# Kernel tuning notes

Hardware: AMD Instinct MI355X
Metric: run time of the kernel (lower is better)

## Reference

```python
import jax, jax.numpy as jnp
import numpy as np

B, T, D = 32, 2048, 128


def setup_inputs() -> dict:
    key = jax.random.key(0)
    k1, k2, k3 = jax.random.split(key, 3)
    values = jax.random.normal(k1, (B, T, D), dtype=jnp.float32)
    # monotonically increasing per-feature timestamps (irregular sampling)
    times = jnp.cumsum(jax.random.uniform(k2, (B, T, D), dtype=jnp.float32), axis=1)
    mask = jax.random.randint(k3, (B, T, D), 0, 2) > 0  # True = observed
    return {"values": values, "times": times, "mask": mask}


def _fill(x, t, mask):
    """Parallel forward fill (LOCF) and backward fill (NOCB) of x and t.

    Replaces the serial Keras RNN scan with cummax/cummin over observation
    indices followed by a gather. Matches ForwardCell semantics:
      forward : x init 0, t init times[:, 0, :]
      backward: x init 0, t init max(times, axis=1)
    """
    Tn = x.shape[1]
    ar = jnp.broadcast_to(jnp.arange(Tn, dtype=jnp.int32)[None, :, None], x.shape)
    # ---- forward fill ----
    fidx = jax.lax.cummax(jnp.where(mask, ar, -1), axis=1)  # last observed idx
    fvalid = fidx >= 0
    fi = jnp.clip(fidx, 0, Tn - 1)
    x_last = jnp.where(fvalid, jnp.take_along_axis(x, fi, axis=1), 0.0)
    t_last = jnp.where(fvalid, jnp.take_along_axis(t, fi, axis=1), t[:, :1, :])
    # ---- backward fill ----
    bidx = jax.lax.cummin(jnp.where(mask, ar, Tn), axis=1, reverse=True)  # next observed idx
    bvalid = bidx < Tn
    bi = jnp.clip(bidx, 0, Tn - 1)
    x_next = jnp.where(bvalid, jnp.take_along_axis(x, bi, axis=1), 0.0)
    t_next = jnp.where(bvalid, jnp.take_along_axis(t, bi, axis=1),
                       jnp.max(t, axis=1, keepdims=True))
    return x_last, t_last, x_next, t_next


def reference(values, times, mask):
    x_last, t_last, x_next, t_next = _fill(values, times, mask)
    denom = t_next - t_last
    num = x_last * (t_next - times) + x_next * (times - t_last)
    safe = denom != 0.0
    x_itp = num / jnp.where(safe, denom, 1.0)
    x_itp = jnp.where(safe & jnp.isfinite(x_itp), x_itp, 0.0)  # nan/inf -> 0
    return jnp.where(mask, values, x_itp)
```

## Files before the change

### kernel.cpp

```cpp
#include <hip/hip_runtime.h>
#include <math.h>

constexpr int B = 32;
constexpr int T = 2048;
constexpr int D = 128;

__global__ __launch_bounds__(256)
void interp_wide_kernel(const float* __restrict__ values,
                        const float* __restrict__ times,
                        const int*   __restrict__ mask,
                        float*       __restrict__ out)
{
    const int gid = blockIdx.x * 256 + threadIdx.x;
    const int d4 = gid & 31;
    const int c  = (gid >> 5) & 511;
    const int b  = gid >> 14;
    const int d0 = d4 << 2;
    const int t0 = c << 2;

    const size_t bbase = (size_t)b * T * D;
    const float* vrow = values + bbase + (size_t)t0 * D + d0;
    const float* trow = times  + bbase + (size_t)t0 * D + d0;
    const int*   mrow = mask   + bbase + (size_t)t0 * D + d0;

    float vv[4][4], tt[4][4];
    unsigned mb[4] = {0u, 0u, 0u, 0u};
#pragma unroll
    for (int i = 0; i < 4; ++i) {
        const float4 a = *reinterpret_cast<const float4*>(vrow + i * D);
        const float4 s = *reinterpret_cast<const float4*>(trow + i * D);
        const int4   m = *reinterpret_cast<const int4*>(mrow + i * D);
        vv[i][0] = a.x; vv[i][1] = a.y; vv[i][2] = a.z; vv[i][3] = a.w;
        tt[i][0] = s.x; tt[i][1] = s.y; tt[i][2] = s.z; tt[i][3] = s.w;
        mb[0] |= (m.x != 0 ? 1u : 0u) << i;
        mb[1] |= (m.y != 0 ? 1u : 0u) << i;
        mb[2] |= (m.z != 0 ? 1u : 0u) << i;
        mb[3] |= (m.w != 0 ? 1u : 0u) << i;
    }

    unsigned fw[4] = {0u, 0u, 0u, 0u};
    unsigned bw[4] = {0u, 0u, 0u, 0u};
#pragma unroll
    for (int k = 0; k < 16; ++k) {
        const int st = t0 - 16 + k;
        if (st >= 0) {
            const int4 m = *reinterpret_cast<const int4*>(
                mask + bbase + (size_t)st * D + d0);
            fw[0] |= (m.x != 0 ? 1u : 0u) << k;
            fw[1] |= (m.y != 0 ? 1u : 0u) << k;
            fw[2] |= (m.z != 0 ? 1u : 0u) << k;
            fw[3] |= (m.w != 0 ? 1u : 0u) << k;
        }
    }
#pragma unroll
    for (int k = 0; k < 16; ++k) {
        const int st = t0 + 4 + k;
        if (st < T) {
            const int4 m = *reinterpret_cast<const int4*>(
                mask + bbase + (size_t)st * D + d0);
            bw[0] |= (m.x != 0 ? 1u : 0u) << k;
            bw[1] |= (m.y != 0 ? 1u : 0u) << k;
            bw[2] |= (m.z != 0 ? 1u : 0u) << k;
            bw[3] |= (m.w != 0 ? 1u : 0u) << k;
        }
    }

    int fi[4], bi[4];
#pragma unroll
    for (int j = 0; j < 4; ++j) {
        fi[j] = fw[j] ? (t0 - 16 + (31 - __builtin_clz(fw[j]))) : -1;
        bi[j] = bw[j] ? (t0 + 4 + __builtin_ctz(bw[j])) : -1;
    }
#pragma unroll
    for (int j = 0; j < 4; ++j) {
        if (fi[j] < 0 && t0 > 16) {
            for (int st = t0 - 17; st >= 0; --st) {
                if (mask[bbase + (size_t)st * D + d0 + j] != 0) { fi[j] = st; break; }
            }
        }
        if (bi[j] < 0 && t0 + 20 < T) {
            for (int st = t0 + 20; st < T; ++st) {
                if (mask[bbase + (size_t)st * D + d0 + j] != 0) { bi[j] = st; break; }
            }
        }
    }

    float fx[4], ft[4], bx[4], bt[4];
#pragma unroll
    for (int j = 0; j < 4; ++j) {
        const int sF = fi[j] < 0 ? 0 : fi[j];
        const int sB = bi[j] < 0 ? 0 : bi[j];
        const size_t oF = bbase + (size_t)sF * D + d0 + j;
        const size_t oB = bbase + (size_t)sB * D + d0 + j;
        fx[j] = values[oF]; ft[j] = times[oF];
        bx[j] = values[oB]; bt[j] = times[oB];
    }
    const float4 tf4 = *reinterpret_cast<const float4*>(times + bbase + d0);
    const float4 tl4 = *reinterpret_cast<const float4*>(
        times + bbase + (size_t)(T - 1) * D + d0);
    const float tfirst[4] = {tf4.x, tf4.y, tf4.z, tf4.w};
    const float tlastT[4] = {tl4.x, tl4.y, tl4.z, tl4.w};
#pragma unroll
    for (int j = 0; j < 4; ++j) {
        if (fi[j] < 0) { fx[j] = 0.f; ft[j] = tfirst[j]; }
        if (bi[j] < 0) { bx[j] = 0.f; bt[j] = tlastT[j]; }
    }

    float res[4][4];
#pragma unroll
    for (int j = 0; j < 4; ++j) {
        float xl[4], tl[4];
        float cfx = fx[j], cft = ft[j];
#pragma unroll
        for (int i = 0; i < 4; ++i) {
            if ((mb[j] >> i) & 1u) { cfx = vv[i][j]; cft = tt[i][j]; }
            xl[i] = cfx; tl[i] = cft;
        }
        float cbx = bx[j], cbt = bt[j];
#pragma unroll
        for (int i = 3; i >= 0; --i) {
            const bool obs = (mb[j] >> i) & 1u;
            if (obs) { cbx = vv[i][j]; cbt = tt[i][j]; }
            const float denom = cbt - tl[i];
            const float num   = xl[i] * (cbt - tt[i][j]) + cbx * (tt[i][j] - tl[i]);
            const bool  safe  = (denom != 0.f);
            float xi = num / (safe ? denom : 1.f);
            xi = (safe && isfinite(xi)) ? xi : 0.f;
            res[i][j] = obs ? vv[i][j] : xi;
        }
    }

    float* orow = out + bbase + (size_t)t0 * D + d0;
#pragma unroll
    for (int i = 0; i < 4; ++i) {
        float4 o; o.x = res[i][0]; o.y = res[i][1]; o.z = res[i][2]; o.w = res[i][3];
        *reinterpret_cast<float4*>(orow + i * D) = o;
    }
}

extern "C" void kernel_launch(void* const* d_in, const int* in_sizes, int n_in,
                              void* d_out, int out_size, void* d_ws, size_t ws_size,
                              hipStream_t stream)
{
    const float* values = (const float*)d_in[0];
    const float* times  = (const float*)d_in[1];
    const int*   mask   = (const int*)d_in[2];
    float*       out    = (float*)d_out;

    const int total_threads = B * (T / 4) * (D / 4);
    interp_wide_kernel<<<total_threads / 256, 256, 0, stream>>>(values, times, mask, out);
}
```

Before: 161.3 us.

## Share halo mask window through LDS bitmasks instead of per-thread global rescans

Each block now covers 32 timesteps by 128 features and loads the mask window, including a 16-step halo on each side, from global memory once. It packs the window into per-feature 64-bit bitmasks in shared memory, and each thread finds its previous and next observation with clz/ctz. Before, every thread reloaded 32 mask rows on its own. The change also drops the separate first/last time loads by gathering directly from index 0 or T-1. In exchange it adds two block barriers and shared-memory traffic.

```diff
diff --git a/kernel.cpp b/kernel.cpp
--- a/kernel.cpp
+++ b/kernel.cpp
@@ -1,109 +1,120 @@
 #include <hip/hip_runtime.h>
 #include <math.h>
 
-constexpr int B = 32;
-constexpr int T = 2048;
-constexpr int D = 128;
+constexpr int B    = 32;
+constexpr int T    = 2048;
+constexpr int D    = 128;
+constexpr int TG   = 32;
+constexpr int HALO = 16;
+constexpr int WIN  = 64;
+constexpr int APAD = 17;
 
 __global__ __launch_bounds__(256)
-void interp_wide_kernel(const float* __restrict__ values,
-                        const float* __restrict__ times,
-                        const int*   __restrict__ mask,
-                        float*       __restrict__ out)
+void interp_lds_kernel(const float* __restrict__ values,
+                       const float* __restrict__ times,
+                       const int*   __restrict__ mask,
+                       float*       __restrict__ out)
 {
-    const int gid = blockIdx.x * 256 + threadIdx.x;
-    const int d4 = gid & 31;
-    const int c  = (gid >> 5) & 511;
-    const int b  = gid >> 14;
-    const int d0 = d4 << 2;
-    const int t0 = c << 2;
+    __shared__ unsigned char A[D * APAD];
+    __shared__ unsigned      W[2][D];
+
+    const int tid   = threadIdx.x;
+    const int blk   = blockIdx.x;
+    const int b     = blk >> 6;
+    const int tg    = blk & 63;
+    const int t_blk = tg * TG;
+    const int w0    = t_blk - HALO;
 
     const size_t bbase = (size_t)b * T * D;
+
+    const int d4    = tid & 31;
+    const int c_loc = tid >> 5;
+    const int d0    = d4 << 2;
+    const int t0    = t_blk + (c_loc << 2);
+
+    float vv[4][4], tt[4][4];
     const float* vrow = values + bbase + (size_t)t0 * D + d0;
     const float* trow = times  + bbase + (size_t)t0 * D + d0;
-    const int*   mrow = mask   + bbase + (size_t)t0 * D + d0;
-
-    float vv[4][4], tt[4][4];
-    unsigned mb[4] = {0u, 0u, 0u, 0u};
 #pragma unroll
     for (int i = 0; i < 4; ++i) {
         const float4 a = *reinterpret_cast<const float4*>(vrow + i * D);
         const float4 s = *reinterpret_cast<const float4*>(trow + i * D);
-        const int4   m = *reinterpret_cast<const int4*>(mrow + i * D);
         vv[i][0] = a.x; vv[i][1] = a.y; vv[i][2] = a.z; vv[i][3] = a.w;
         tt[i][0] = s.x; tt[i][1] = s.y; tt[i][2] = s.z; tt[i][3] = s.w;
-        mb[0] |= (m.x != 0 ? 1u : 0u) << i;
-        mb[1] |= (m.y != 0 ? 1u : 0u) << i;
-        mb[2] |= (m.z != 0 ? 1u : 0u) << i;
-        mb[3] |= (m.w != 0 ? 1u : 0u) << i;
     }
 
-    unsigned fw[4] = {0u, 0u, 0u, 0u};
-    unsigned bw[4] = {0u, 0u, 0u, 0u};
 #pragma unroll
-    for (int k = 0; k < 16; ++k) {
-        const int st = t0 - 16 + k;
-        if (st >= 0) {
-            const int4 m = *reinterpret_cast<const int4*>(
-                mask + bbase + (size_t)st * D + d0);
-            fw[0] |= (m.x != 0 ? 1u : 0u) << k;
-            fw[1] |= (m.y != 0 ? 1u : 0u) << k;
-            fw[2] |= (m.z != 0 ? 1u : 0u) << k;
-            fw[3] |= (m.w != 0 ? 1u : 0u) << k;
+    for (int k = 0; k < 2; ++k) {
+        const int task = tid + k * 256;
+        const int td4  = task & 31;
+        const int ts4  = task >> 5;
+        const int tdd  = td4 << 2;
+        unsigned n0 = 0, n1 = 0, n2 = 0, n3 = 0;
+#pragma unroll
+        for (int i = 0; i < 4; ++i) {
+            const int st = w0 + (ts4 << 2) + i;
+            if (st >= 0 && st < T) {
+                const int4 m = *reinterpret_cast<const int4*>(
+                    mask + bbase + (size_t)st * D + tdd);
+                n0 |= (m.x != 0 ? 1u : 0u) << i;
+                n1 |= (m.y != 0 ? 1u : 0u) << i;
+                n2 |= (m.z != 0 ? 1u : 0u) << i;
+                n3 |= (m.w != 0 ? 1u : 0u) << i;
+            }
         }
+        A[(tdd + 0) * APAD + ts4] = (unsigned char)n0;
+        A[(tdd + 1) * APAD + ts4] = (unsigned char)n1;
+        A[(tdd + 2) * APAD + ts4] = (unsigned char)n2;
+        A[(tdd + 3) * APAD + ts4] = (unsigned char)n3;
     }
+    __syncthreads();
+
+    {
+        const int r = tid & 127;
+        const int h = tid >> 7;
+        unsigned acc = 0;
 #pragma unroll
-    for (int k = 0; k < 16; ++k) {
-        const int st = t0 + 4 + k;
-        if (st < T) {
-            const int4 m = *reinterpret_cast<const int4*>(
-                mask + bbase + (size_t)st * D + d0);
-            bw[0] |= (m.x != 0 ? 1u : 0u) << k;
-            bw[1] |= (m.y != 0 ? 1u : 0u) << k;
-            bw[2] |= (m.z != 0 ? 1u : 0u) << k;
-            bw[3] |= (m.w != 0 ? 1u : 0u) << k;
-        }
+        for (int q = 0; q < 8; ++q)
+            acc |= (unsigned)(A[r * APAD + (h << 3) + q] & 0xF) << (q << 2);
+        W[h][r] = acc;
     }
+    __syncthreads();
 
+    const int pos = HALO + (c_loc << 2);
     int fi[4], bi[4];
+    unsigned mb[4];
 #pragma unroll
     for (int j = 0; j < 4; ++j) {
-        fi[j] = fw[j] ? (t0 - 16 + (31 - __builtin_clz(fw[j]))) : -1;
-        bi[j] = bw[j] ? (t0 + 4 + __builtin_ctz(bw[j])) : -1;
-    }
-#pragma unroll
-    for (int j = 0; j < 4; ++j) {
-        if (fi[j] < 0 && t0 > 16) {
-            for (int st = t0 - 17; st >= 0; --st) {
+        const unsigned long long w =
+            ((unsigned long long)W[1][d0 + j] << 32) | (unsigned long long)W[0][d0 + j];
+        mb[j] = (unsigned)((w >> pos) & 0xFull);
+        const unsigned long long below = w & ((1ull << pos) - 1ull);
+        const unsigned long long above = w >> (pos + 4);
+        fi[j] = below ? (w0 + 63 - __builtin_clzll(below)) : -1;
+        bi[j] = above ? (t0 + 4 + __builtin_ctzll(above)) : -1;
+        if (fi[j] < 0 && w0 > 0) {
+            for (int st = w0 - 1; st >= 0; --st)
                 if (mask[bbase + (size_t)st * D + d0 + j] != 0) { fi[j] = st; break; }
-            }
         }
-        if (bi[j] < 0 && t0 + 20 < T) {
-            for (int st = t0 + 20; st < T; ++st) {
+        if (bi[j] < 0 && w0 + WIN < T) {
+            for (int st = w0 + WIN; st < T; ++st)
                 if (mask[bbase + (size_t)st * D + d0 + j] != 0) { bi[j] = st; break; }
-            }
         }
     }
 
     float fx[4], ft[4], bx[4], bt[4];
 #pragma unroll
     for (int j = 0; j < 4; ++j) {
-        const int sF = fi[j] < 0 ? 0 : fi[j];
-        const int sB = bi[j] < 0 ? 0 : bi[j];
+        const int sF = (fi[j] >= 0) ? fi[j] : 0;
+        const int sB = (bi[j] >= 0) ? bi[j] : (T - 1);
         const size_t oF = bbase + (size_t)sF * D + d0 + j;
         const size_t oB = bbase + (size_t)sB * D + d0 + j;
-        fx[j] = values[oF]; ft[j] = times[oF];
-        bx[j] = values[oB]; bt[j] = times[oB];
-    }
-    const float4 tf4 = *reinterpret_cast<const float4*>(times + bbase + d0);
-    const float4 tl4 = *reinterpret_cast<const float4*>(
-        times + bbase + (size_t)(T - 1) * D + d0);
-    const float tfirst[4] = {tf4.x, tf4.y, tf4.z, tf4.w};
-    const float tlastT[4] = {tl4.x, tl4.y, tl4.z, tl4.w};
-#pragma unroll
-    for (int j = 0; j < 4; ++j) {
-        if (fi[j] < 0) { fx[j] = 0.f; ft[j] = tfirst[j]; }
-        if (bi[j] < 0) { bx[j] = 0.f; bt[j] = tlastT[j]; }
+        const float lvF = values[oF], ltF = times[oF];
+        const float lvB = values[oB], ltB = times[oB];
+        fx[j] = (fi[j] >= 0) ? lvF : 0.f;
+        ft[j] = ltF;
+        bx[j] = (bi[j] >= 0) ? lvB : 0.f;
+        bt[j] = ltB;
     }
 
     float res[4][4];
@@ -147,6 +158,6 @@
     const int*   mask   = (const int*)d_in[2];
     float*       out    = (float*)d_out;
 
-    const int total_threads = B * (T / 4) * (D / 4);
-    interp_wide_kernel<<<total_threads / 256, 256, 0, stream>>>(values, times, mask, out);
+    const int blocks = B * (T / TG);
+    interp_lds_kernel<<<blocks, 256, 0, stream>>>(values, times, mask, out);
 }
```

Result: faster. 147.8 us (-8.4%).

## Share per-row boundary observations via LDS to eliminate redundant halo mask reads

Applied to the files above, without the earlier changes.

Each block now covers 64 timesteps with 8 row groups of 8 steps. Each group publishes its last and first observed value and time plus its mask bits to shared memory. Neighbouring groups look up fill values there instead of re-reading a 32-row mask halo per thread. Global halo scans happen only at block edges, which removes most redundant mask traffic. The cost is a block-wide barrier, more registers per thread and half as many threads.

```diff
diff --git a/kernel.cpp b/kernel.cpp
--- a/kernel.cpp
+++ b/kernel.cpp
@@ -1,32 +1,46 @@
 #include <hip/hip_runtime.h>
 #include <math.h>
 
-constexpr int B = 32;
-constexpr int T = 2048;
-constexpr int D = 128;
+constexpr int B   = 32;
+constexpr int T   = 2048;
+constexpr int D   = 128;
+constexpr int CS  = 8;
+constexpr int RT  = 8;
+constexpr int BT  = RT * CS;
+constexpr int PAD = 129;
 
 __global__ __launch_bounds__(256)
-void interp_wide_kernel(const float* __restrict__ values,
+void interp_xchg_kernel(const float* __restrict__ values,
                         const float* __restrict__ times,
                         const int*   __restrict__ mask,
                         float*       __restrict__ out)
 {
-    const int gid = blockIdx.x * 256 + threadIdx.x;
-    const int d4 = gid & 31;
-    const int c  = (gid >> 5) & 511;
-    const int b  = gid >> 14;
-    const int d0 = d4 << 2;
-    const int t0 = c << 2;
+    __shared__ float    SLV[RT][PAD];
+    __shared__ float    SLT[RT][PAD];
+    __shared__ float    SFV[RT][PAD];
+    __shared__ float    SFT[RT][PAD];
+    __shared__ unsigned SM [RT][PAD];
+
+    const int tid = threadIdx.x;
+    const int d4  = tid & 31;
+    const int row = tid >> 5;
+    const int d0  = d4 << 2;
+
+    const int blk = blockIdx.x;
+    const int b   = blk >> 5;
+    const int tb  = blk & 31;
+    const int bt0 = tb * BT;
+    const int t0  = bt0 + row * CS;
 
     const size_t bbase = (size_t)b * T * D;
     const float* vrow = values + bbase + (size_t)t0 * D + d0;
     const float* trow = times  + bbase + (size_t)t0 * D + d0;
     const int*   mrow = mask   + bbase + (size_t)t0 * D + d0;
 
-    float vv[4][4], tt[4][4];
+    float vv[CS][4], tt[CS][4];
     unsigned mb[4] = {0u, 0u, 0u, 0u};
 #pragma unroll
-    for (int i = 0; i < 4; ++i) {
+    for (int i = 0; i < CS; ++i) {
         const float4 a = *reinterpret_cast<const float4*>(vrow + i * D);
         const float4 s = *reinterpret_cast<const float4*>(trow + i * D);
         const int4   m = *reinterpret_cast<const int4*>(mrow + i * D);
@@ -38,91 +52,108 @@
         mb[3] |= (m.w != 0 ? 1u : 0u) << i;
     }
 
-    unsigned fw[4] = {0u, 0u, 0u, 0u};
-    unsigned bw[4] = {0u, 0u, 0u, 0u};
+    unsigned pb[4] = {0u, 0u, 0u, 0u};
+    unsigned nb[4] = {0u, 0u, 0u, 0u};
+    if (row == 0 && bt0 > 0) {
 #pragma unroll
-    for (int k = 0; k < 16; ++k) {
-        const int st = t0 - 16 + k;
-        if (st >= 0) {
+        for (int k = 0; k < 16; ++k) {
+            const int st = bt0 - 16 + k;
             const int4 m = *reinterpret_cast<const int4*>(
                 mask + bbase + (size_t)st * D + d0);
-            fw[0] |= (m.x != 0 ? 1u : 0u) << k;
-            fw[1] |= (m.y != 0 ? 1u : 0u) << k;
-            fw[2] |= (m.z != 0 ? 1u : 0u) << k;
-            fw[3] |= (m.w != 0 ? 1u : 0u) << k;
+            pb[0] |= (m.x != 0 ? 1u : 0u) << k;
+            pb[1] |= (m.y != 0 ? 1u : 0u) << k;
+            pb[2] |= (m.z != 0 ? 1u : 0u) << k;
+            pb[3] |= (m.w != 0 ? 1u : 0u) << k;
         }
     }
+    if (row == RT - 1 && bt0 + BT < T) {
 #pragma unroll
-    for (int k = 0; k < 16; ++k) {
-        const int st = t0 + 4 + k;
-        if (st < T) {
+        for (int k = 0; k < 16; ++k) {
+            const int st = bt0 + BT + k;
             const int4 m = *reinterpret_cast<const int4*>(
                 mask + bbase + (size_t)st * D + d0);
-            bw[0] |= (m.x != 0 ? 1u : 0u) << k;
-            bw[1] |= (m.y != 0 ? 1u : 0u) << k;
-            bw[2] |= (m.z != 0 ? 1u : 0u) << k;
-            bw[3] |= (m.w != 0 ? 1u : 0u) << k;
+            nb[0] |= (m.x != 0 ? 1u : 0u) << k;
+            nb[1] |= (m.y != 0 ? 1u : 0u) << k;
+            nb[2] |= (m.z != 0 ? 1u : 0u) << k;
+            nb[3] |= (m.w != 0 ? 1u : 0u) << k;
         }
     }
 
-    int fi[4], bi[4];
 #pragma unroll
     for (int j = 0; j < 4; ++j) {
-        fi[j] = fw[j] ? (t0 - 16 + (31 - __builtin_clz(fw[j]))) : -1;
-        bi[j] = bw[j] ? (t0 + 4 + __builtin_ctz(bw[j])) : -1;
+        float lv = 0.f, lt = 0.f, fv = 0.f, ft = 0.f;
+#pragma unroll
+        for (int i = 0; i < CS; ++i)
+            if ((mb[j] >> i) & 1u) { lv = vv[i][j]; lt = tt[i][j]; }
+#pragma unroll
+        for (int i = CS - 1; i >= 0; --i)
+            if ((mb[j] >> i) & 1u) { fv = vv[i][j]; ft = tt[i][j]; }
+        const int d = d0 + j;
+        SLV[row][d] = lv; SLT[row][d] = lt;
+        SFV[row][d] = fv; SFT[row][d] = ft;
+        SM [row][d] = mb[j];
     }
+    __syncthreads();
+
+    float res[CS][4];
 #pragma unroll
     for (int j = 0; j < 4; ++j) {
-        if (fi[j] < 0 && t0 > 16) {
-            for (int st = t0 - 17; st >= 0; --st) {
-                if (mask[bbase + (size_t)st * D + d0 + j] != 0) { fi[j] = st; break; }
+        const int d = d0 + j;
+
+        float cfx = 0.f, cft = 0.f;
+        bool have = false;
+        for (int r = row - 1; r >= 0; --r) {
+            if (SM[r][d]) { cfx = SLV[r][d]; cft = SLT[r][d]; have = true; break; }
+        }
+        if (!have && pb[j]) {
+            const int st = bt0 - 16 + (31 - __builtin_clz(pb[j]));
+            const size_t o = bbase + (size_t)st * D + d;
+            cfx = values[o]; cft = times[o]; have = true;
+        }
+        if (!have) {
+            const int start = (row == 0) ? (bt0 - 17) : (bt0 - 1);
+            for (int st = start; st >= 0; --st) {
+                if (mask[bbase + (size_t)st * D + d] != 0) {
+                    const size_t o = bbase + (size_t)st * D + d;
+                    cfx = values[o]; cft = times[o]; have = true; break;
+                }
             }
         }
-        if (bi[j] < 0 && t0 + 20 < T) {
-            for (int st = t0 + 20; st < T; ++st) {
-                if (mask[bbase + (size_t)st * D + d0 + j] != 0) { bi[j] = st; break; }
+        if (!have) { cfx = 0.f; cft = times[bbase + d]; }
+
+        float cbx = 0.f, cbt = 0.f;
+        bool haveb = false;
+        for (int r = row + 1; r < RT; ++r) {
+            if (SM[r][d]) { cbx = SFV[r][d]; cbt = SFT[r][d]; haveb = true; break; }
+        }
+        if (!haveb && nb[j]) {
+            const int st = bt0 + BT + __builtin_ctz(nb[j]);
+            const size_t o = bbase + (size_t)st * D + d;
+            cbx = values[o]; cbt = times[o]; haveb = true;
+        }
+        if (!haveb) {
+            const int start = bt0 + BT + ((row == RT - 1) ? 16 : 0);
+            for (int st = start; st < T; ++st) {
+                if (mask[bbase + (size_t)st * D + d] != 0) {
+                    const size_t o = bbase + (size_t)st * D + d;
+                    cbx = values[o]; cbt = times[o]; haveb = true; break;
+                }
             }
         }
-    }
+        if (!haveb) { cbx = 0.f; cbt = times[bbase + (size_t)(T - 1) * D + d]; }
 
-    float fx[4], ft[4], bx[4], bt[4];
+        float xl[CS], tl_[CS];
 #pragma unroll
-    for (int j = 0; j < 4; ++j) {
-        const int sF = fi[j] < 0 ? 0 : fi[j];
-        const int sB = bi[j] < 0 ? 0 : bi[j];
-        const size_t oF = bbase + (size_t)sF * D + d0 + j;
-        const size_t oB = bbase + (size_t)sB * D + d0 + j;
-        fx[j] = values[oF]; ft[j] = times[oF];
-        bx[j] = values[oB]; bt[j] = times[oB];
-    }
-    const float4 tf4 = *reinterpret_cast<const float4*>(times + bbase + d0);
-    const float4 tl4 = *reinterpret_cast<const float4*>(
-        times + bbase + (size_t)(T - 1) * D + d0);
-    const float tfirst[4] = {tf4.x, tf4.y, tf4.z, tf4.w};
-    const float tlastT[4] = {tl4.x, tl4.y, tl4.z, tl4.w};
+        for (int i = 0; i < CS; ++i) {
+            if ((mb[j] >> i) & 1u) { cfx = vv[i][j]; cft = tt[i][j]; }
+            xl[i] = cfx; tl_[i] = cft;
+        }
 #pragma unroll
-    for (int j = 0; j < 4; ++j) {
-        if (fi[j] < 0) { fx[j] = 0.f; ft[j] = tfirst[j]; }
-        if (bi[j] < 0) { bx[j] = 0.f; bt[j] = tlastT[j]; }
-    }
-
-    float res[4][4];
-#pragma unroll
-    for (int j = 0; j < 4; ++j) {
-        float xl[4], tl[4];
-        float cfx = fx[j], cft = ft[j];
-#pragma unroll
-        for (int i = 0; i < 4; ++i) {
-            if ((mb[j] >> i) & 1u) { cfx = vv[i][j]; cft = tt[i][j]; }
-            xl[i] = cfx; tl[i] = cft;
-        }
-        float cbx = bx[j], cbt = bt[j];
-#pragma unroll
-        for (int i = 3; i >= 0; --i) {
+        for (int i = CS - 1; i >= 0; --i) {
             const bool obs = (mb[j] >> i) & 1u;
             if (obs) { cbx = vv[i][j]; cbt = tt[i][j]; }
-            const float denom = cbt - tl[i];
-            const float num   = xl[i] * (cbt - tt[i][j]) + cbx * (tt[i][j] - tl[i]);
+            const float denom = cbt - tl_[i];
+            const float num   = xl[i] * (cbt - tt[i][j]) + cbx * (tt[i][j] - tl_[i]);
             const bool  safe  = (denom != 0.f);
             float xi = num / (safe ? denom : 1.f);
             xi = (safe && isfinite(xi)) ? xi : 0.f;
@@ -132,7 +163,7 @@
 
     float* orow = out + bbase + (size_t)t0 * D + d0;
 #pragma unroll
-    for (int i = 0; i < 4; ++i) {
+    for (int i = 0; i < CS; ++i) {
         float4 o; o.x = res[i][0]; o.y = res[i][1]; o.z = res[i][2]; o.w = res[i][3];
         *reinterpret_cast<float4*>(orow + i * D) = o;
     }
@@ -147,6 +178,6 @@
     const int*   mask   = (const int*)d_in[2];
     float*       out    = (float*)d_out;
 
-    const int total_threads = B * (T / 4) * (D / 4);
-    interp_wide_kernel<<<total_threads / 256, 256, 0, stream>>>(values, times, mask, out);
+    const int blocks = B * (T / BT);
+    interp_xchg_kernel<<<blocks, 256, 0, stream>>>(values, times, mask, out);
 }
```

Result: faster. 145.1 us (-10.1%).
